# Performance work log

Measured on AMD Instinct MI355X. Metric: run time of the kernel, lower is better.

The kernel has to match this reference:

```python
import jax, jax.numpy as jnp
import numpy as np

B, IN, H = 4096, 1024, 1024


def setup_inputs() -> dict:
    key = jax.random.key(0)
    ks = jax.random.split(key, 6)
    s_h = 1.0 / np.sqrt(H)
    s_x = 1.0 / np.sqrt(IN)
    return {
        "x": jax.random.normal(ks[0], (B, IN), jnp.float32),
        "h": jax.random.normal(ks[1], (B, H), jnp.float32),
        "c": jax.random.normal(ks[2], (B, H), jnp.float32),
        # hidden_lin: Linear(H, 4H) with bias
        "Wh": jax.random.uniform(ks[3], (4 * H, H), jnp.float32, -s_h, s_h),
        "bh": jax.random.uniform(ks[4], (4 * H,), jnp.float32, -s_h, s_h),
        # input_lin: Linear(IN, 4H), bias=False
        "Wx": jax.random.uniform(ks[5], (4 * H, IN), jnp.float32, -s_x, s_x),
    }


def reference(x, h, c, Wh, bh, Wx):
    # ifgo = h @ Wh^T + bh + x @ Wx^T   -> [B, 4H]
    ifgo = jnp.dot(h, Wh.T) + bh + jnp.dot(x, Wx.T)
    i, f, g, o = jnp.split(ifgo, 4, axis=1)
    i = jax.nn.sigmoid(i)
    f = jax.nn.sigmoid(f)
    g = jnp.tanh(g)
    o = jax.nn.sigmoid(o)
    c_next = f * c + i * g
    h_next = o * jnp.tanh(c_next)
    return (h_next, c_next)
```

## Files before the change

### kernel.cpp

```cpp
#include <hip/hip_runtime.h>
#include <cstdint>
#include <cstddef>


#define NB   4096
#define KH   1024
#define KK   2048
#define ARR_ELEMS 4194304
#define NKT  32

typedef __bf16 bf16x8 __attribute__((ext_vector_type(8)));
typedef float  f32x4  __attribute__((ext_vector_type(4)));

__device__ inline unsigned short f2bf(float f) {
    union { float f; unsigned int u; } v; v.f = f;
    unsigned int u = v.u;
    u += 0x7FFFu + ((u >> 16) & 1u);
    return (unsigned short)(u >> 16);
}

__device__ inline float fsig(float v)  { return __builtin_amdgcn_rcpf(1.f + __expf(-v)); }
__device__ inline float ftanh(float v) { return 1.f - 2.f * __builtin_amdgcn_rcpf(1.f + __expf(2.f * v)); }

__global__ void convert_kernel(const float* __restrict__ h, const float* __restrict__ x,
                               const float* __restrict__ Wh, const float* __restrict__ Wx,
                               unsigned short* __restrict__ A, unsigned short* __restrict__ W) {
    int idx = blockIdx.x * 256 + threadIdx.x;
    int arr = idx >> 20;
    int off = (idx & 0xFFFFF) << 2;
    const float* src = (arr == 0) ? h : (arr == 1) ? x : (arr == 2) ? Wh : Wx;
    float4 v = *(const float4*)(src + off);
    unsigned int lo = (unsigned int)f2bf(v.x) | ((unsigned int)f2bf(v.y) << 16);
    unsigned int hi = (unsigned int)f2bf(v.z) | ((unsigned int)f2bf(v.w) << 16);
    uint2 packed; packed.x = lo; packed.y = hi;

    int row = off >> 10;
    int col = off & 1023;
    unsigned short* dst;
    size_t dstOff;
    if (arr < 2) {
        dst = A;
        dstOff = (size_t)row * KK + (arr == 1 ? 1024 : 0) + col;
    } else {
        int g = row >> 10, j = row & 1023;
        int p = ((j >> 4) << 6) | (g << 4) | (j & 15);
        dst = W;
        dstOff = (size_t)p * KK + (arr == 3 ? 1024 : 0) + col;
    }
    *(uint2*)(dst + dstOff) = packed;
}

__global__ __launch_bounds__(512, 2) void gemm_kernel(const unsigned short* __restrict__ A,
                            const unsigned short* __restrict__ W,
                            const float* __restrict__ bh,
                            const float* __restrict__ c,
                            float* __restrict__ out) {
    __shared__ __align__(16) unsigned short As[2 * 16384];
    __shared__ __align__(16) unsigned short Bs[2 * 16384];

    const int tid  = threadIdx.x;
    const int wave = tid >> 6;
    const int lane = tid & 63;

    const int bid   = (int)blockIdx.x;
    const int swz   = (bid & 7) * 32 + (bid >> 3);
    const int tileM = swz >> 4;
    const int tileN = swz & 15;

    const int wr  = wave >> 2;
    const int wc  = wave & 3;
    const int fr  = lane & 15;
    const int fk2 = (lane >> 4) << 4;

    const unsigned short* pa[4];
    const unsigned short* pb[4];
    #pragma unroll
    for (int i = 0; i < 4; ++i) {
        const int P   = (i * 512 + tid) * 16;
        const int L   = P ^ (((P >> 7) & 7) << 4);
        const int row = L >> 7;
        const int kk  = (L & 127) >> 1;
        pa[i] = A + (size_t)(tileM * 256 + row) * KK + kk;
        pb[i] = W + (size_t)(tileN * 256 + row) * KK + kk;
    }

    const int swzm = (fr & 7) << 4;
    int offA[8], offB[4];
    #pragma unroll
    for (int i = 0; i < 8; ++i)
        offA[i] = (wr * 128 + i * 16 + fr) * 128 + (fk2 ^ swzm);
    #pragma unroll
    for (int j = 0; j < 4; ++j)
        offB[j] = (wc * 64 + j * 16 + fr) * 128 + (fk2 ^ swzm);

    f32x4 acc[8][4] = {};
    bf16x8 afr[4][2], bfr[4][2];

#define STAGE(KT, BUF) do { \
    const size_t _ko = (size_t)(KT) * 64; \
    _Pragma("unroll") \
    for (int _i = 0; _i < 4; ++_i) { \
        __builtin_amdgcn_global_load_lds( \
            (const __attribute__((address_space(1))) void*)(pa[_i] + _ko), \
            (__attribute__((address_space(3))) void*)(As + (BUF) * 16384 + _i * 4096 + wave * 512), 16, 0, 0); \
        __builtin_amdgcn_global_load_lds( \
            (const __attribute__((address_space(1))) void*)(pb[_i] + _ko), \
            (__attribute__((address_space(3))) void*)(Bs + (BUF) * 16384 + _i * 4096 + wave * 512), 16, 0, 0); \
    } \
} while (0)

#define MFMA16(IB, JB) do { \
    _Pragma("unroll") \
    for (int _i = 0; _i < 4; ++_i) \
        _Pragma("unroll") \
        for (int _j = 0; _j < 2; ++_j) \
            _Pragma("unroll") \
            for (int _s = 0; _s < 2; ++_s) \
                acc[(IB) + _i][(JB) + _j] = __builtin_amdgcn_mfma_f32_16x16x32_bf16( \
                    afr[_i][_s], bfr[(JB) + _j][_s], acc[(IB) + _i][(JB) + _j], 0, 0, 0); \
} while (0)

    STAGE(0, 0);
    STAGE(1, 1);
    asm volatile("s_waitcnt vmcnt(8)" ::: "memory");
    asm volatile("s_barrier" ::: "memory");

#define TILE(T, BUF) do { \
    const char* AsB = (const char*)As + (BUF) * 32768; \
    const char* BsB = (const char*)Bs + (BUF) * 32768; \
     \
    _Pragma("unroll") \
    for (int i = 0; i < 4; ++i) { \
        afr[i][0] = *(const bf16x8*)(AsB + offA[i]); \
        afr[i][1] = *(const bf16x8*)(AsB + (offA[i] ^ 64)); \
    } \
    _Pragma("unroll") \
    for (int j = 0; j < 2; ++j) { \
        bfr[j][0] = *(const bf16x8*)(BsB + offB[j]); \
        bfr[j][1] = *(const bf16x8*)(BsB + (offB[j] ^ 64)); \
    } \
    asm volatile("s_barrier" ::: "memory"); \
    asm volatile("s_waitcnt lgkmcnt(0)" ::: "memory"); \
    __builtin_amdgcn_s_setprio(1); \
    MFMA16(0, 0); \
    __builtin_amdgcn_s_setprio(0); \
    asm volatile("s_barrier" ::: "memory"); \
     \
    _Pragma("unroll") \
    for (int j = 2; j < 4; ++j) { \
        bfr[j][0] = *(const bf16x8*)(BsB + offB[j]); \
        bfr[j][1] = *(const bf16x8*)(BsB + (offB[j] ^ 64)); \
    } \
    asm volatile("s_barrier" ::: "memory"); \
    asm volatile("s_waitcnt lgkmcnt(0)" ::: "memory"); \
    __builtin_amdgcn_s_setprio(1); \
    MFMA16(0, 2); \
    __builtin_amdgcn_s_setprio(0); \
    asm volatile("s_barrier" ::: "memory"); \
     \
    _Pragma("unroll") \
    for (int i = 0; i < 4; ++i) { \
        afr[i][0] = *(const bf16x8*)(AsB + offA[4 + i]); \
        afr[i][1] = *(const bf16x8*)(AsB + (offA[4 + i] ^ 64)); \
    } \
    asm volatile("s_barrier" ::: "memory"); \
    asm volatile("s_waitcnt lgkmcnt(0)" ::: "memory"); \
    __builtin_amdgcn_s_setprio(1); \
    MFMA16(4, 0); \
    __builtin_amdgcn_s_setprio(0); \
    asm volatile("s_barrier" ::: "memory"); \
     \
    { \
        const int _ktc = ((T) + 2 <= NKT - 1) ? ((T) + 2) : (NKT - 1); \
        STAGE(_ktc, BUF);  \
    } \
    asm volatile("s_barrier" ::: "memory"); \
    __builtin_amdgcn_s_setprio(1); \
    MFMA16(4, 2); \
    __builtin_amdgcn_s_setprio(0); \
    asm volatile("s_waitcnt vmcnt(8)" ::: "memory"); \
    asm volatile("s_barrier" ::: "memory"); \
} while (0)

    for (int tt = 0; tt < NKT; tt += 2) {
        TILE(tt, 0);
        TILE(tt + 1, 1);
    }
#undef TILE
#undef MFMA16
#undef STAGE

    const int j = ((tileN * 4 + wc) << 4) | fr;
    const float bi  = bh[j];
    const float bff = bh[j + 1024];
    const float bg  = bh[j + 2048];
    const float bo  = bh[j + 3072];

    const int row0 = tileM * 256 + wr * 128 + (lane >> 4) * 4;

    float cv[8][4];
    #pragma unroll
    for (int i = 0; i < 8; ++i)
        #pragma unroll
        for (int r = 0; r < 4; ++r)
            cv[i][r] = c[(size_t)(row0 + i * 16 + r) * KH + j];

    #pragma unroll
    for (int i = 0; i < 8; ++i) {
        #pragma unroll
        for (int r = 0; r < 4; ++r) {
            const size_t idx = (size_t)(row0 + i * 16 + r) * KH + j;
            float iv = fsig(acc[i][0][r] + bi);
            float fv = fsig(acc[i][1][r] + bff);
            float gv = ftanh(acc[i][2][r] + bg);
            float ov = fsig(acc[i][3][r] + bo);
            float cn = fv * cv[i][r] + iv * gv;
            float hn = ov * ftanh(cn);
            out[idx] = hn;
            out[(size_t)ARR_ELEMS + idx] = cn;
        }
    }
}

extern "C" void kernel_launch(void* const* d_in, const int* in_sizes, int n_in,
                              void* d_out, int out_size, void* d_ws, size_t ws_size,
                              hipStream_t stream) {
    const float* x  = (const float*)d_in[0];
    const float* h  = (const float*)d_in[1];
    const float* c  = (const float*)d_in[2];
    const float* Wh = (const float*)d_in[3];
    const float* bh = (const float*)d_in[4];
    const float* Wx = (const float*)d_in[5];
    float* out = (float*)d_out;

    unsigned short* ws   = (unsigned short*)d_ws;
    unsigned short* Acat = ws;
    unsigned short* Wcat = ws + 2 * (size_t)ARR_ELEMS;

    convert_kernel<<<16384, 256, 0, stream>>>(h, x, Wh, Wx, Acat, Wcat);
    gemm_kernel<<<256, 512, 0, stream>>>(Acat, Wcat, bh, c, out);
}
```

Measured before the change: 196.4 us.

## Restructure GEMM K-tile schedule with split fragment registers and fewer barriers

The GEMM inner tile now keeps separate register sets for the two A halves and two B halves. All A fragments and half of B are loaded up front, and three MFMA quadrants run before a single barrier and the next stage prefetch, replacing the previous schedule with many barriers per tile. Separately, the convert kernel now handles 8 floats per thread with 16-byte stores and launches half as many blocks. The new schedule holds more live fragment registers, which may pressure occupancy under launch_bounds(512,2), and it changes how LDS reads are ordered against the async global-to-LDS stores.

```diff
diff --git a/kernel.cpp b/kernel.cpp
--- a/kernel.cpp
+++ b/kernel.cpp
@@ -26,13 +26,16 @@
                                const float* __restrict__ Wh, const float* __restrict__ Wx,
                                unsigned short* __restrict__ A, unsigned short* __restrict__ W) {
     int idx = blockIdx.x * 256 + threadIdx.x;
-    int arr = idx >> 20;
-    int off = (idx & 0xFFFFF) << 2;
+    int arr = idx >> 19;
+    int off = (idx & 0x7FFFF) << 3;
     const float* src = (arr == 0) ? h : (arr == 1) ? x : (arr == 2) ? Wh : Wx;
-    float4 v = *(const float4*)(src + off);
-    unsigned int lo = (unsigned int)f2bf(v.x) | ((unsigned int)f2bf(v.y) << 16);
-    unsigned int hi = (unsigned int)f2bf(v.z) | ((unsigned int)f2bf(v.w) << 16);
-    uint2 packed; packed.x = lo; packed.y = hi;
+    float4 v0 = *(const float4*)(src + off);
+    float4 v1 = *(const float4*)(src + off + 4);
+    uint4 packed;
+    packed.x = (unsigned int)f2bf(v0.x) | ((unsigned int)f2bf(v0.y) << 16);
+    packed.y = (unsigned int)f2bf(v0.z) | ((unsigned int)f2bf(v0.w) << 16);
+    packed.z = (unsigned int)f2bf(v1.x) | ((unsigned int)f2bf(v1.y) << 16);
+    packed.w = (unsigned int)f2bf(v1.z) | ((unsigned int)f2bf(v1.w) << 16);
 
     int row = off >> 10;
     int col = off & 1023;
@@ -47,7 +50,7 @@
         dst = W;
         dstOff = (size_t)p * KK + (arr == 3 ? 1024 : 0) + col;
     }
-    *(uint2*)(dst + dstOff) = packed;
+    *(uint4*)(dst + dstOff) = packed;
 }
 
 __global__ __launch_bounds__(512, 2) void gemm_kernel(const unsigned short* __restrict__ A,
@@ -94,7 +97,7 @@
         offB[j] = (wc * 64 + j * 16 + fr) * 128 + (fk2 ^ swzm);
 
     f32x4 acc[8][4] = {};
-    bf16x8 afr[4][2], bfr[4][2];
+    bf16x8 a03[4][2], a47[4][2], b01[2][2], b23[2][2];
 
 #define STAGE(KT, BUF) do { \
     const size_t _ko = (size_t)(KT) * 64; \
@@ -109,7 +112,24 @@
     } \
 } while (0)
 
-#define MFMA16(IB, JB) do { \
+#define READ_A(dst, base, AsB) do { \
+    _Pragma("unroll") \
+    for (int _i = 0; _i < 4; ++_i) { \
+        dst[_i][0] = *(const bf16x8*)((AsB) + offA[(base) + _i]); \
+        dst[_i][1] = *(const bf16x8*)((AsB) + (offA[(base) + _i] ^ 64)); \
+    } \
+} while (0)
+
+#define READ_B(dst, base, BsB) do { \
+    _Pragma("unroll") \
+    for (int _j = 0; _j < 2; ++_j) { \
+        dst[_j][0] = *(const bf16x8*)((BsB) + offB[(base) + _j]); \
+        dst[_j][1] = *(const bf16x8*)((BsB) + (offB[(base) + _j] ^ 64)); \
+    } \
+} while (0)
+
+#define MFMAQ(af, bf, IB, JB) do { \
+    __builtin_amdgcn_s_setprio(1); \
     _Pragma("unroll") \
     for (int _i = 0; _i < 4; ++_i) \
         _Pragma("unroll") \
@@ -117,7 +137,29 @@
             _Pragma("unroll") \
             for (int _s = 0; _s < 2; ++_s) \
                 acc[(IB) + _i][(JB) + _j] = __builtin_amdgcn_mfma_f32_16x16x32_bf16( \
-                    afr[_i][_s], bfr[(JB) + _j][_s], acc[(IB) + _i][(JB) + _j], 0, 0, 0); \
+                    af[_i][_s], bf[_j][_s], acc[(IB) + _i][(JB) + _j], 0, 0, 0); \
+    __builtin_amdgcn_s_setprio(0); \
+} while (0)
+
+#define TILEBODY(T, BUF) do { \
+    const char* AsB = (const char*)As + (BUF) * 32768; \
+    const char* BsB = (const char*)Bs + (BUF) * 32768; \
+    READ_B(b01, 0, BsB); \
+    READ_A(a03, 0, AsB); \
+    READ_A(a47, 4, AsB); \
+    MFMAQ(a03, b01, 0, 0); \
+    READ_B(b23, 2, BsB); \
+    MFMAQ(a47, b01, 4, 0); \
+    MFMAQ(a47, b23, 4, 2); \
+    asm volatile("s_waitcnt lgkmcnt(0)" ::: "memory"); \
+    asm volatile("s_barrier" ::: "memory"); \
+    { \
+        const int _kt = ((T) + 2 <= NKT - 1) ? ((T) + 2) : (NKT - 1); \
+        STAGE(_kt, BUF);    \
+    } \
+    asm volatile("s_waitcnt vmcnt(8)" ::: "memory"); \
+    asm volatile("s_barrier" ::: "memory"); \
+    MFMAQ(a03, b23, 0, 2); \
 } while (0)
 
     STAGE(0, 0);
@@ -125,69 +167,14 @@
     asm volatile("s_waitcnt vmcnt(8)" ::: "memory");
     asm volatile("s_barrier" ::: "memory");
 
-#define TILE(T, BUF) do { \
-    const char* AsB = (const char*)As + (BUF) * 32768; \
-    const char* BsB = (const char*)Bs + (BUF) * 32768; \
-     \
-    _Pragma("unroll") \
-    for (int i = 0; i < 4; ++i) { \
-        afr[i][0] = *(const bf16x8*)(AsB + offA[i]); \
-        afr[i][1] = *(const bf16x8*)(AsB + (offA[i] ^ 64)); \
-    } \
-    _Pragma("unroll") \
-    for (int j = 0; j < 2; ++j) { \
-        bfr[j][0] = *(const bf16x8*)(BsB + offB[j]); \
-        bfr[j][1] = *(const bf16x8*)(BsB + (offB[j] ^ 64)); \
-    } \
-    asm volatile("s_barrier" ::: "memory"); \
-    asm volatile("s_waitcnt lgkmcnt(0)" ::: "memory"); \
-    __builtin_amdgcn_s_setprio(1); \
-    MFMA16(0, 0); \
-    __builtin_amdgcn_s_setprio(0); \
-    asm volatile("s_barrier" ::: "memory"); \
-     \
-    _Pragma("unroll") \
-    for (int j = 2; j < 4; ++j) { \
-        bfr[j][0] = *(const bf16x8*)(BsB + offB[j]); \
-        bfr[j][1] = *(const bf16x8*)(BsB + (offB[j] ^ 64)); \
-    } \
-    asm volatile("s_barrier" ::: "memory"); \
-    asm volatile("s_waitcnt lgkmcnt(0)" ::: "memory"); \
-    __builtin_amdgcn_s_setprio(1); \
-    MFMA16(0, 2); \
-    __builtin_amdgcn_s_setprio(0); \
-    asm volatile("s_barrier" ::: "memory"); \
-     \
-    _Pragma("unroll") \
-    for (int i = 0; i < 4; ++i) { \
-        afr[i][0] = *(const bf16x8*)(AsB + offA[4 + i]); \
-        afr[i][1] = *(const bf16x8*)(AsB + (offA[4 + i] ^ 64)); \
-    } \
-    asm volatile("s_barrier" ::: "memory"); \
-    asm volatile("s_waitcnt lgkmcnt(0)" ::: "memory"); \
-    __builtin_amdgcn_s_setprio(1); \
-    MFMA16(4, 0); \
-    __builtin_amdgcn_s_setprio(0); \
-    asm volatile("s_barrier" ::: "memory"); \
-     \
-    { \
-        const int _ktc = ((T) + 2 <= NKT - 1) ? ((T) + 2) : (NKT - 1); \
-        STAGE(_ktc, BUF);  \
-    } \
-    asm volatile("s_barrier" ::: "memory"); \
-    __builtin_amdgcn_s_setprio(1); \
-    MFMA16(4, 2); \
-    __builtin_amdgcn_s_setprio(0); \
-    asm volatile("s_waitcnt vmcnt(8)" ::: "memory"); \
-    asm volatile("s_barrier" ::: "memory"); \
-} while (0)
-
     for (int tt = 0; tt < NKT; tt += 2) {
-        TILE(tt, 0);
-        TILE(tt + 1, 1);
-    }
-#undef TILE
-#undef MFMA16
+        TILEBODY(tt, 0);
+        TILEBODY(tt + 1, 1);
+    }
+#undef TILEBODY
+#undef MFMAQ
+#undef READ_A
+#undef READ_B
 #undef STAGE
 
     const int j = ((tileN * 4 + wc) << 4) | fr;
@@ -237,6 +224,6 @@
     unsigned short* Acat = ws;
     unsigned short* Wcat = ws + 2 * (size_t)ARR_ELEMS;
 
-    convert_kernel<<<16384, 256, 0, stream>>>(h, x, Wh, Wx, Acat, Wcat);
+    convert_kernel<<<8192, 256, 0, stream>>>(h, x, Wh, Wx, Acat, Wcat);
     gemm_kernel<<<256, 512, 0, stream>>>(Acat, Wcat, bh, c, out);
 }
```

After: 194.8 us. About the same (-0.8%).
